# Optimization experiments

Measured on AMD Instinct MI355X. Metric: run time of the kernel, lower is better.

## Reference

```python
import jax, jax.numpy as jnp
import numpy as np

B, P, ENC, DEC, ATT = 256, 196, 2048, 512, 512


def setup_inputs() -> dict:
    key = jax.random.key(0)
    ks = jax.random.split(key, 8)
    s_enc = 1.0 / np.sqrt(ENC)
    s_dec = 1.0 / np.sqrt(DEC)
    s_att = 1.0 / np.sqrt(ATT)
    return {
        "encoder_out": jax.random.normal(ks[0], (B, P, ENC), jnp.float32),
        "decoder_hidden": jax.random.normal(ks[1], (B, DEC), jnp.float32),
        "W_enc": jax.random.uniform(ks[2], (ENC, ATT), jnp.float32, -s_enc, s_enc),
        "b_enc": jax.random.uniform(ks[3], (ATT,), jnp.float32, -s_enc, s_enc),
        "W_dec": jax.random.uniform(ks[4], (DEC, ATT), jnp.float32, -s_dec, s_dec),
        "b_dec": jax.random.uniform(ks[5], (ATT,), jnp.float32, -s_dec, s_dec),
        "W_full": jax.random.uniform(ks[6], (ATT,), jnp.float32, -s_att, s_att),
        "b_full": jax.random.uniform(ks[7], (), jnp.float32, -s_att, s_att),
    }


def reference(encoder_out, decoder_hidden, W_enc, b_enc, W_dec, b_dec, W_full, b_full):
    # att1: [B, P, ATT]; att2: [B, ATT]
    att1 = jnp.einsum("bpe,ea->bpa", encoder_out, W_enc) + b_enc
    att2 = decoder_hidden @ W_dec + b_dec
    # additive combine + relu + scalar projection -> [B, P]
    att = jnp.einsum("bpa,a->bp", jax.nn.relu(att1 + att2[:, None, :]), W_full) + b_full
    alpha = jax.nn.softmax(att, axis=1)  # softmax over pixels
    context_vector = jnp.einsum("bpe,bp->be", encoder_out, alpha)
    return (context_vector, alpha)
```

## Files before the change

### kernel.cpp

```cpp
#include <hip/hip_runtime.h>
#include <stdint.h>


using u16x8 = __attribute__((ext_vector_type(8))) unsigned short;
using s16x8 = __attribute__((ext_vector_type(8))) short;
using f32x4 = __attribute__((ext_vector_type(4))) float;

typedef __attribute__((address_space(1))) const void gvoid_t;
typedef __attribute__((address_space(3))) void lvoid_t;

static __device__ __forceinline__ unsigned short f2b(float f) {
  unsigned int u = __builtin_bit_cast(unsigned int, f);
  u = u + 0x7fffu + ((u >> 16) & 1u);
  return (unsigned short)(u >> 16);
}

static __device__ __forceinline__ void glds16(const void* g, void* l) {
  __builtin_amdgcn_global_load_lds((gvoid_t*)g, (lvoid_t*)l, 16, 0, 0);
}

__global__ __launch_bounds__(256) void transpose_wenc(
    const float* __restrict__ wenc, unsigned short* __restrict__ wencT) {
  const int g = blockIdx.x * 256 + threadIdx.x;
  const int ks = g >> 11;
  const int c = g & 2047;
  const int n = c >> 2;
  const int kc = c & 3;
  const float* src = wenc + (size_t)(ks * 32 + kc * 8) * 512 + n;
  u16x8 v;
#pragma unroll
  for (int j = 0; j < 8; ++j) v[j] = f2b(src[(size_t)j * 512]);
  const int idx = (n * 32 + kc * 8) ^ ((n & 7) << 3);
  *(u16x8*)&wencT[(size_t)ks * 16384 + idx] = v;
}

__global__ __launch_bounds__(256) void comb_kernel(
    const float* __restrict__ dec, const float* __restrict__ wdec,
    const float* __restrict__ bdec, const float* __restrict__ benc,
    float* __restrict__ comb) {
  __shared__ float dec_sh[512];
  const int b = blockIdx.x, t = threadIdx.x;
  dec_sh[t] = dec[(size_t)b * 512 + t];
  dec_sh[256 + t] = dec[(size_t)b * 512 + 256 + t];
  __syncthreads();
  const int a0 = 2 * t;
  float acc0 = bdec[a0] + benc[a0];
  float acc1 = bdec[a0 + 1] + benc[a0 + 1];
#pragma unroll 8
  for (int e = 0; e < 512; ++e) {
    float2 wv = *(const float2*)&wdec[(size_t)e * 512 + a0];
    float d = dec_sh[e];
    acc0 = fmaf(d, wv.x, acc0);
    acc1 = fmaf(d, wv.y, acc1);
  }
  *(float2*)&comb[(size_t)b * 512 + a0] = make_float2(acc0, acc1);
}

__global__ __launch_bounds__(512, 4) void gemm_att(
    const float* __restrict__ enc, const unsigned short* __restrict__ wencT,
    const float* __restrict__ comb, const float* __restrict__ wfull_g,
    float* __restrict__ att) {
  __shared__ alignas(16) unsigned short Bsh[2][16384];
  __shared__ alignas(16) unsigned short Ash[2][2048];
  __shared__ float comb_sh[1024];
  __shared__ float wfull_sh[512];
  __shared__ float att_sh[64];

  const int t = threadIdx.x;
  const int l = t & 63;
  const int quad = l >> 4, col = l & 15;
  const int w = t >> 6;
  const int wm = w >> 2, wn = w & 3;
  const int r0 = blockIdx.x * 64;
  const int b0 = r0 / 196;
  const int rsw = (b0 + 1) * 196;
  const int b1 = (b0 + 1 < 256) ? b0 + 1 : 255;

  comb_sh[t] = comb[(size_t)b0 * 512 + t];
  comb_sh[512 + t] = comb[(size_t)b1 * 512 + t];
  wfull_sh[t] = wfull_g[t];
  if (t < 64) att_sh[t] = 0.0f;

  const int arow = (t & 255) >> 2, achk = t & 3;
  const float* ap = enc + (size_t)(r0 + arow) * 2048 + achk * 8;
  const int a_lds = (arow * 32 + achk * 8) ^ ((arow & 7) << 3);

  const unsigned short* bgp[4];
  int blds[4];
#pragma unroll
  for (int j = 0; j < 4; ++j) {
    const int c = j * 512 + t;
    bgp[j] = wencT + (size_t)c * 8;
    blds[j] = c * 8;
  }

  int aoff[2], boff[8];
#pragma unroll
  for (int mt = 0; mt < 2; ++mt) {
    const int row = wm * 32 + mt * 16 + col;
    aoff[mt] = (row * 32 + quad * 8) ^ ((row & 7) << 3);
  }
#pragma unroll
  for (int nt = 0; nt < 8; ++nt) {
    const int n = wn * 128 + nt * 16 + col;
    boff[nt] = (n * 32 + quad * 8) ^ ((n & 7) << 3);
  }

  f32x4 acc[2][8];
#pragma unroll
  for (int mt = 0; mt < 2; ++mt)
#pragma unroll
    for (int nt = 0; nt < 8; ++nt) acc[mt][nt] = (f32x4){0.f, 0.f, 0.f, 0.f};

#pragma unroll
  for (int j = 0; j < 4; ++j) {
    glds16(bgp[j], &Bsh[0][blds[j]]);
    bgp[j] += 16384;
  }
  if (t < 256) {
    f32x4 a0v = *(const f32x4*)ap;
    f32x4 a1v = *(const f32x4*)(ap + 4);
    u16x8 av;
    av[0] = f2b(a0v[0]); av[1] = f2b(a0v[1]); av[2] = f2b(a0v[2]); av[3] = f2b(a0v[3]);
    av[4] = f2b(a1v[0]); av[5] = f2b(a1v[1]); av[6] = f2b(a1v[2]); av[7] = f2b(a1v[3]);
    *(u16x8*)&Ash[0][a_lds] = av;
  }
  ap += 32;
  __syncthreads();

#pragma unroll 2
  for (int ks = 0; ks < 64; ++ks) {
    const int buf = ks & 1, nbuf = buf ^ 1;
    const bool pf = (ks < 63);

    f32x4 a0v, a1v;
    if (pf && t < 256) {
      a0v = *(const f32x4*)ap;
      a1v = *(const f32x4*)(ap + 4);
    }
    __builtin_amdgcn_sched_barrier(0);
    if (pf) {
#pragma unroll
      for (int j = 0; j < 4; ++j) {
        glds16(bgp[j], &Bsh[nbuf][blds[j]]);
        bgp[j] += 16384;
      }
    }
    __builtin_amdgcn_sched_barrier(0);

    s16x8 afr0 = *(const s16x8*)&Ash[buf][aoff[0]];
    s16x8 afr1 = *(const s16x8*)&Ash[buf][aoff[1]];
#pragma unroll
    for (int nt = 0; nt < 8; ++nt) {
      s16x8 bfr = *(const s16x8*)&Bsh[buf][boff[nt]];
      acc[0][nt] = __builtin_amdgcn_mfma_f32_16x16x32_bf16(afr0, bfr, acc[0][nt], 0, 0, 0);
      acc[1][nt] = __builtin_amdgcn_mfma_f32_16x16x32_bf16(afr1, bfr, acc[1][nt], 0, 0, 0);
    }
    __builtin_amdgcn_sched_barrier(0);

    if (pf && t < 256) {
      u16x8 av;
      av[0] = f2b(a0v[0]); av[1] = f2b(a0v[1]); av[2] = f2b(a0v[2]); av[3] = f2b(a0v[3]);
      av[4] = f2b(a1v[0]); av[5] = f2b(a1v[1]); av[6] = f2b(a1v[2]); av[7] = f2b(a1v[3]);
      *(u16x8*)&Ash[nbuf][a_lds] = av;
      ap += 32;
    }
    __builtin_amdgcn_sched_barrier(0);
    asm volatile("s_waitcnt vmcnt(0) lgkmcnt(0)" ::: "memory");
    __builtin_amdgcn_sched_barrier(0);
    __builtin_amdgcn_s_barrier();
  }

  __syncthreads();
#pragma unroll
  for (int mt = 0; mt < 2; ++mt) {
#pragma unroll
    for (int r = 0; r < 4; ++r) {
      const int rl = wm * 32 + mt * 16 + quad * 4 + r;
      const int cb = ((r0 + rl) >= rsw) ? 512 : 0;
      float s = 0.f;
#pragma unroll
      for (int nt = 0; nt < 8; ++nt) {
        const int n = wn * 128 + nt * 16 + col;
        float v = acc[mt][nt][r] + comb_sh[cb + n];
        v = fmaxf(v, 0.f);
        s = fmaf(v, wfull_sh[n], s);
      }
      s += __shfl_xor(s, 1);
      s += __shfl_xor(s, 2);
      s += __shfl_xor(s, 4);
      s += __shfl_xor(s, 8);
      if (col == 0) atomicAdd(&att_sh[rl], s);
    }
  }
  __syncthreads();
  if (t < 64) att[(size_t)r0 + t] = att_sh[t];
}

__global__ __launch_bounds__(256) void softmax_ctx(
    const float* __restrict__ att, const float* __restrict__ enc,
    float* __restrict__ ctx_out, float* __restrict__ alpha_out) {
  const int b = blockIdx.x >> 1, slice = blockIdx.x & 1;
  const int t = threadIdx.x;
  __shared__ float red[256];
  __shared__ float alpha_sh[196];

  float v = (t < 196) ? att[(size_t)b * 196 + t] : -1e30f;
  red[t] = v;
  __syncthreads();
  for (int s = 128; s > 0; s >>= 1) {
    if (t < s) red[t] = fmaxf(red[t], red[t + s]);
    __syncthreads();
  }
  float mx = red[0];
  __syncthreads();
  float e = (t < 196) ? __expf(v - mx) : 0.f;
  red[t] = e;
  __syncthreads();
  for (int s = 128; s > 0; s >>= 1) {
    if (t < s) red[t] += red[t + s];
    __syncthreads();
  }
  float a = e / red[0];
  if (t < 196) {
    alpha_sh[t] = a;
    if (slice == 0) alpha_out[(size_t)b * 196 + t] = a;
  }
  __syncthreads();

  f32x4 acc = {0.f, 0.f, 0.f, 0.f};
  const float* ep = enc + (size_t)b * 196 * 2048 + slice * 1024 + t * 4;
#pragma unroll 4
  for (int p = 0; p < 196; ++p) {
    float ap = alpha_sh[p];
    f32x4 ev = *(const f32x4*)ep;
    acc[0] = fmaf(ap, ev[0], acc[0]);
    acc[1] = fmaf(ap, ev[1], acc[1]);
    acc[2] = fmaf(ap, ev[2], acc[2]);
    acc[3] = fmaf(ap, ev[3], acc[3]);
    ep += 2048;
  }
  *(f32x4*)(ctx_out + (size_t)b * 2048 + slice * 1024 + t * 4) = acc;
}

extern "C" void kernel_launch(void* const* d_in, const int* in_sizes, int n_in,
                              void* d_out, int out_size, void* d_ws, size_t ws_size,
                              hipStream_t stream) {
  (void)in_sizes; (void)n_in; (void)out_size; (void)ws_size;
  const float* enc   = (const float*)d_in[0];
  const float* dec   = (const float*)d_in[1];
  const float* wenc  = (const float*)d_in[2];
  const float* benc  = (const float*)d_in[3];
  const float* wdec  = (const float*)d_in[4];
  const float* bdec  = (const float*)d_in[5];
  const float* wfull = (const float*)d_in[6];

  unsigned short* wencT = (unsigned short*)d_ws;
  float* comb = (float*)((char*)d_ws + (2u << 20));
  float* att  = (float*)((char*)d_ws + (2u << 20) + (512u << 10));

  float* ctx_out = (float*)d_out;
  float* alpha_out = ctx_out + (size_t)256 * 2048;

  hipLaunchKernelGGL(transpose_wenc, dim3(512), dim3(256), 0, stream, wenc, wencT);
  hipLaunchKernelGGL(comb_kernel, dim3(256), dim3(256), 0, stream, dec, wdec, bdec, benc, comb);
  hipLaunchKernelGGL(gemm_att, dim3(784), dim3(512), 0, stream, enc, wencT, comb, wfull, att);
  hipLaunchKernelGGL(softmax_ctx, dim3(512), dim3(256), 0, stream, att, enc, ctx_out, alpha_out);
}
```

Baseline: 734.7 us.

## Deepen A-tile prefetch to two stages and spread loads across all threads

The A-tile load of encoder rows now uses all 512 threads, each loading one float4 instead of 256 threads loading two. A register-held prefetch two K-steps ahead lets the wait before the barrier keep one global load in flight (vmcnt(1)) rather than draining everything. The loop peels its last iteration and raises wave priority around the MFMA block. The aim is to hide global-load latency on the fp32 encoder stream. It adds register pressure and relies on exact vmcnt ordering between the LDS-direct B loads and the A register loads.

```diff
diff --git a/kernel.cpp b/kernel.cpp
--- a/kernel.cpp
+++ b/kernel.cpp
@@ -3,6 +3,7 @@
 
 
 using u16x8 = __attribute__((ext_vector_type(8))) unsigned short;
+using u16x4 = __attribute__((ext_vector_type(4))) unsigned short;
 using s16x8 = __attribute__((ext_vector_type(8))) short;
 using f32x4 = __attribute__((ext_vector_type(4))) float;
 
@@ -81,9 +82,9 @@
   wfull_sh[t] = wfull_g[t];
   if (t < 64) att_sh[t] = 0.0f;
 
-  const int arow = (t & 255) >> 2, achk = t & 3;
-  const float* ap = enc + (size_t)(r0 + arow) * 2048 + achk * 8;
-  const int a_lds = (arow * 32 + achk * 8) ^ ((arow & 7) << 3);
+  const int arow = t >> 3, ak4 = t & 7;
+  const float* ap = enc + (size_t)(r0 + arow) * 2048 + ak4 * 4;
+  const int a_lds = (arow * 32 + ak4 * 4) ^ ((arow & 7) << 3);
 
   const unsigned short* bgp[4];
   int blds[4];
@@ -117,58 +118,70 @@
     glds16(bgp[j], &Bsh[0][blds[j]]);
     bgp[j] += 16384;
   }
-  if (t < 256) {
-    f32x4 a0v = *(const f32x4*)ap;
-    f32x4 a1v = *(const f32x4*)(ap + 4);
-    u16x8 av;
+  f32x4 a0v = *(const f32x4*)ap;
+  ap += 32;
+  f32x4 a_hold = *(const f32x4*)ap;
+  ap += 32;
+  {
+    u16x4 av;
     av[0] = f2b(a0v[0]); av[1] = f2b(a0v[1]); av[2] = f2b(a0v[2]); av[3] = f2b(a0v[3]);
-    av[4] = f2b(a1v[0]); av[5] = f2b(a1v[1]); av[6] = f2b(a1v[2]); av[7] = f2b(a1v[3]);
-    *(u16x8*)&Ash[0][a_lds] = av;
-  }
-  ap += 32;
-  __syncthreads();
-
-#pragma unroll 2
-  for (int ks = 0; ks < 64; ++ks) {
+    *(u16x4*)&Ash[0][a_lds] = av;
+  }
+  __syncthreads();
+
+  for (int ks = 0; ks < 63; ++ks) {
     const int buf = ks & 1, nbuf = buf ^ 1;
-    const bool pf = (ks < 63);
-
-    f32x4 a0v, a1v;
-    if (pf && t < 256) {
-      a0v = *(const f32x4*)ap;
-      a1v = *(const f32x4*)(ap + 4);
-    }
-    __builtin_amdgcn_sched_barrier(0);
-    if (pf) {
-#pragma unroll
-      for (int j = 0; j < 4; ++j) {
-        glds16(bgp[j], &Bsh[nbuf][blds[j]]);
-        bgp[j] += 16384;
-      }
-    }
-    __builtin_amdgcn_sched_barrier(0);
-
-    s16x8 afr0 = *(const s16x8*)&Ash[buf][aoff[0]];
-    s16x8 afr1 = *(const s16x8*)&Ash[buf][aoff[1]];
+
+#pragma unroll
+    for (int j = 0; j < 4; ++j) {
+      glds16(bgp[j], &Bsh[nbuf][blds[j]]);
+      bgp[j] += 16384;
+    }
+    __builtin_amdgcn_sched_barrier(0);
+
+    f32x4 a_new = *(const f32x4*)ap;
+    if (ks < 61) ap += 32;
+    __builtin_amdgcn_sched_barrier(0);
+
+    const unsigned short* Ab = &Ash[buf][0];
+    const unsigned short* Bb = &Bsh[buf][0];
+    s16x8 afr0 = *(const s16x8*)(Ab + aoff[0]);
+    s16x8 afr1 = *(const s16x8*)(Ab + aoff[1]);
+    __builtin_amdgcn_s_setprio(1);
 #pragma unroll
     for (int nt = 0; nt < 8; ++nt) {
-      s16x8 bfr = *(const s16x8*)&Bsh[buf][boff[nt]];
+      s16x8 bfr = *(const s16x8*)(Bb + boff[nt]);
       acc[0][nt] = __builtin_amdgcn_mfma_f32_16x16x32_bf16(afr0, bfr, acc[0][nt], 0, 0, 0);
       acc[1][nt] = __builtin_amdgcn_mfma_f32_16x16x32_bf16(afr1, bfr, acc[1][nt], 0, 0, 0);
     }
-    __builtin_amdgcn_sched_barrier(0);
-
-    if (pf && t < 256) {
-      u16x8 av;
-      av[0] = f2b(a0v[0]); av[1] = f2b(a0v[1]); av[2] = f2b(a0v[2]); av[3] = f2b(a0v[3]);
-      av[4] = f2b(a1v[0]); av[5] = f2b(a1v[1]); av[6] = f2b(a1v[2]); av[7] = f2b(a1v[3]);
-      *(u16x8*)&Ash[nbuf][a_lds] = av;
-      ap += 32;
-    }
-    __builtin_amdgcn_sched_barrier(0);
-    asm volatile("s_waitcnt vmcnt(0) lgkmcnt(0)" ::: "memory");
+    __builtin_amdgcn_s_setprio(0);
+    __builtin_amdgcn_sched_barrier(0);
+
+    {
+      u16x4 av;
+      av[0] = f2b(a_hold[0]); av[1] = f2b(a_hold[1]);
+      av[2] = f2b(a_hold[2]); av[3] = f2b(a_hold[3]);
+      *(u16x4*)&Ash[nbuf][a_lds] = av;
+    }
+    a_hold = a_new;
+    __builtin_amdgcn_sched_barrier(0);
+
+    asm volatile("s_waitcnt vmcnt(1) lgkmcnt(0)" ::: "memory");
     __builtin_amdgcn_sched_barrier(0);
     __builtin_amdgcn_s_barrier();
+  }
+
+  {
+    const unsigned short* Ab = &Ash[1][0];
+    const unsigned short* Bb = &Bsh[1][0];
+    s16x8 afr0 = *(const s16x8*)(Ab + aoff[0]);
+    s16x8 afr1 = *(const s16x8*)(Ab + aoff[1]);
+#pragma unroll
+    for (int nt = 0; nt < 8; ++nt) {
+      s16x8 bfr = *(const s16x8*)(Bb + boff[nt]);
+      acc[0][nt] = __builtin_amdgcn_mfma_f32_16x16x32_bf16(afr0, bfr, acc[0][nt], 0, 0, 0);
+      acc[1][nt] = __builtin_amdgcn_mfma_f32_16x16x32_bf16(afr1, bfr, acc[1][nt], 0, 0, 0);
+    }
   }
 
   __syncthreads();
```

After: 726.2 us. Within noise of the previous version (-1.2%).
